# Kernel optimization log

Measured on AMD Instinct MI355X. Metric: run time of the kernel, lower is better.

The kernel has to match this reference:

```python
import jax, jax.numpy as jnp
import numpy as np

N, E, G = 20000, 200000, 32
D, H, C, L = 384, 12, 32, 6
NUM_RBF = 100
RBF_MIN, RBF_MAX = 0.0, 30.0


def _layer_norm(x, g, b, eps=1e-5):
    mu = jnp.mean(x, axis=-1, keepdims=True)
    var = jnp.var(x, axis=-1, keepdims=True)
    return (x - mu) * jax.lax.rsqrt(var + eps) * g + b


def setup_inputs() -> dict:
    key = jax.random.key(0)
    ks = jax.random.split(key, 32)
    s = 0.05
    inp = {
        'x': jax.random.normal(ks[0], (N, 20), jnp.float32),
        'pos': jax.random.normal(ks[1], (N, 3), jnp.float32) * 10.0,
        'edge_index': jax.random.randint(ks[2], (2, E), 0, N),
        'batch': jnp.sort(jax.random.randint(ks[3], (N,), 0, G)),
        # node embedding: Linear(20,384) + LayerNorm
        'emb_W': jax.random.normal(ks[4], (20, D)) * s,
        'emb_b': jnp.zeros((D,)),
        'emb_g': jnp.ones((D,)),
        'emb_beta': jnp.zeros((D,)),
        # edge encoder: Linear(100,384), Linear(384,384), LayerNorm
        'eW1': jax.random.normal(ks[5], (NUM_RBF, D)) * s,
        'eb1': jnp.zeros((D,)),
        'eW2': jax.random.normal(ks[6], (D, D)) * s,
        'eb2': jnp.zeros((D,)),
        'e_g': jnp.ones((D,)),
        'e_beta': jnp.zeros((D,)),
        # 6 stacked GATv2 layers
        'Wl': jax.random.normal(ks[7], (L, D, D)) * s,
        'bl': jnp.zeros((L, D)),
        'Wr': jax.random.normal(ks[8], (L, D, D)) * s,
        'br': jnp.zeros((L, D)),
        'We': jax.random.normal(ks[9], (L, D, D)) * s,
        'att': jax.random.normal(ks[10], (L, H, C)) * s,
        'cb': jnp.zeros((L, D)),
        # BatchNorm (eval mode, running stats)
        'bn_g': 1.0 + jax.random.normal(ks[11], (L, D)) * 0.05,
        'bn_b': jax.random.normal(ks[12], (L, D)) * 0.05,
        'bn_m': jax.random.normal(ks[13], (L, D)) * 0.05,
        'bn_v': jax.random.uniform(ks[14], (L, D), minval=0.5, maxval=1.5),
        # pool combine + head
        'pW': jax.random.normal(ks[15], (2 * D, D)) * s,
        'pb': jnp.zeros((D,)),
        'hW1': jax.random.normal(ks[16], (D, D)) * s,
        'hb1': jnp.zeros((D,)),
        'hW2': jax.random.normal(ks[17], (D, D // 2)) * s,
        'hb2': jnp.zeros((D // 2,)),
        'hW3': jax.random.normal(ks[18], (D // 2, 1)) * s,
        'hb3': jnp.zeros((1,)),
    }
    return inp


def reference(x, pos, edge_index, batch, emb_W, emb_b, emb_g, emb_beta,
              eW1, eb1, eW2, eb2, e_g, e_beta,
              Wl, bl, Wr, br, We, att, cb, bn_g, bn_b, bn_m, bn_v,
              pW, pb, hW1, hb1, hW2, hb2, hW3, hb3):
    src, dst = edge_index[0], edge_index[1]

    # node embedding (dropout = identity in eval)
    h = jax.nn.silu(_layer_norm(x @ emb_W + emb_b, emb_g, emb_beta))  # (N, D)

    # RBF edge features
    centers = jnp.linspace(RBF_MIN, RBF_MAX, NUM_RBF)
    spacing = (RBF_MAX - RBF_MIN) / (NUM_RBF - 1)
    gamma = 1.0 / (spacing ** 2 + 1e-8)
    dist = jnp.linalg.norm(pos[src] - pos[dst], axis=-1, keepdims=True)  # (E, 1)
    rbf = jnp.exp(-gamma * (dist - centers) ** 2)  # (E, NUM_RBF)
    e = jax.nn.silu(rbf @ eW1 + eb1)
    e = _layer_norm(e @ eW2 + eb2, e_g, e_beta)  # (E, D)

    for i in range(L):
        identity = h
        xl = (h @ Wl[i] + bl[i]).reshape(N, H, C)
        xr = (h @ Wr[i] + br[i]).reshape(N, H, C)
        ee = (e @ We[i]).reshape(E, H, C)
        m = jax.nn.leaky_relu(xl[src] + xr[dst] + ee, 0.2)  # (E, H, C)
        logits = jnp.einsum('ehc,hc->eh', m, att[i])  # (E, H)
        smax = jax.ops.segment_max(logits, dst, num_segments=N)
        a = jnp.exp(logits - smax[dst])
        denom = jax.ops.segment_sum(a, dst, num_segments=N)
        a = a / (denom[dst] + 1e-16)
        msg = (xl[src] * a[:, :, None]).reshape(E, H * C)
        out = jax.ops.segment_sum(msg, dst, num_segments=N) + cb[i]  # (N, D)
        out = (out - bn_m[i]) * jax.lax.rsqrt(bn_v[i] + 1e-5) * bn_g[i] + bn_b[i]
        h = jax.nn.silu(out) + identity

    cnt = jax.ops.segment_sum(jnp.ones((N,), h.dtype), batch, num_segments=G)
    h_mean = jax.ops.segment_sum(h, batch, num_segments=G) / jnp.maximum(cnt, 1.0)[:, None]
    h_max = jax.ops.segment_max(h, batch, num_segments=G)
    hg = jnp.concatenate([h_mean, h_max], axis=-1)  # (G, 2D)
    hg = jax.nn.silu(hg @ pW + pb)
    hg = jax.nn.silu(hg @ hW1 + hb1)
    hg = jax.nn.silu(hg @ hW2 + hb2)
    return (hg @ hW3 + hb3).squeeze(-1)  # (G,)
```

## Files before the change

### kernel.cpp

```cpp
#include <hip/hip_runtime.h>
#include <hip/hip_bf16.h>
#include <math.h>

#define NN 20000
#define EE 200000
#define GG 32
#define DD 384
#define HH 12
#define CC 32
#define LL 6
#define NRBF 100
#define CHUNK 32768

typedef short s16x8 __attribute__((ext_vector_type(8)));
typedef float f32x4 __attribute__((ext_vector_type(4)));
typedef unsigned int u32;

__device__ __forceinline__ float siluf(float x) { return x / (1.f + __expf(-x)); }
__device__ __forceinline__ float bf2f(unsigned short u) {
    return __uint_as_float(((unsigned int)u) << 16);
}

__device__ __forceinline__ void atomicMaxF(float* addr, float val) {
    if (val >= 0.f) atomicMax((int*)addr, __float_as_int(val));
    else atomicMin((unsigned int*)addr, __float_as_uint(val));
}

__device__ __forceinline__ void gload16(const void* g, void* l) {
    __builtin_amdgcn_global_load_lds((const __attribute__((address_space(1))) u32*)g,
                                     (__attribute__((address_space(3))) u32*)l, 16, 0, 0);
}

__device__ __forceinline__ bool tile_decode(int NC, int nrows, int& rowt, int& col) {
    const int t = blockIdx.x;
    const int q = t >> 3;
    col = q % NC;
    rowt = (q / NC) * 8 + (t & 7);
    return rowt < nrows;
}

__global__ void EquivariantProteinGNN_45552423141948_kernel() {}

__device__ __forceinline__ void gemm_kloop(const __hip_bfloat16* __restrict__ A,
                                           const __hip_bfloat16* __restrict__ Bt,
                                           int M, int K, int m0, int n0,
                                           unsigned short* As, unsigned short* Bs,
                                           f32x4 (&acc)[4][4]) {
    char* AsB = (char*)As;
    char* BsB = (char*)Bs;
    const int t = threadIdx.x;
    const int w = t >> 6, l = t & 63;
    const int wr = w >> 1, wc = w & 1;

    const int seg0 = 2 * w, seg1 = seg0 + 1;
    const int r0s = seg0 * 16 + (l >> 2);
    const int r1s = seg1 * 16 + (l >> 2);
    const int cg0 = (l & 3) ^ ((r0s >> 1) & 3);
    const int cg1 = (l & 3) ^ ((r1s >> 1) & 3);
    const size_t aSrc0 = (size_t)min(m0 + r0s, M - 1) * K + cg0 * 8;
    const size_t aSrc1 = (size_t)min(m0 + r1s, M - 1) * K + cg1 * 8;
    const size_t bSrc0 = (size_t)(n0 + r0s) * K + cg0 * 8;
    const size_t bSrc1 = (size_t)(n0 + r1s) * K + cg1 * 8;
    unsigned short* AsW0 = As + seg0 * 512;
    unsigned short* AsW1 = As + seg1 * 512;
    unsigned short* BsW0 = Bs + seg0 * 512;
    unsigned short* BsW1 = Bs + seg1 * 512;

    int aoff[4], boff[4];
#pragma unroll
    for (int m = 0; m < 4; ++m) {
        const int row = wr * 64 + m * 16 + (l & 15);
        aoff[m] = row * 64 + ((((l >> 4)) ^ ((row >> 1) & 3)) << 4);
        const int rowb = wc * 64 + m * 16 + (l & 15);
        boff[m] = rowb * 64 + ((((l >> 4)) ^ ((rowb >> 1) & 3)) << 4);
    }

    for (int kk = 0; kk < K; kk += 32) {
        __syncthreads();
        gload16(A + aSrc0 + kk, AsW0);
        gload16(A + aSrc1 + kk, AsW1);
        gload16(Bt + bSrc0 + kk, BsW0);
        gload16(Bt + bSrc1 + kk, BsW1);
        __syncthreads();
        s16x8 af[4], bfr[4];
#pragma unroll
        for (int m = 0; m < 4; ++m) af[m] = *(const s16x8*)(AsB + aoff[m]);
#pragma unroll
        for (int n = 0; n < 4; ++n) bfr[n] = *(const s16x8*)(BsB + boff[n]);
#pragma unroll
        for (int m = 0; m < 4; ++m)
#pragma unroll
            for (int n = 0; n < 4; ++n)
                acc[m][n] = __builtin_amdgcn_mfma_f32_16x16x32_bf16(af[m], bfr[n], acc[m][n], 0, 0, 0);
    }
}

template<bool BIAS, bool SILU>
__global__ __launch_bounds__(256) void k_gemm_bt(const __hip_bfloat16* __restrict__ A,
                                                 const __hip_bfloat16* __restrict__ Bt,
                                                 const float* __restrict__ bias,
                                                 __hip_bfloat16* __restrict__ Cmat,
                                                 int M, int N, int K) {
    int rowt, colt;
    if (!tile_decode(N >> 7, (M + 127) >> 7, rowt, colt)) return;
    const int m0 = rowt << 7, n0 = colt << 7;

    __shared__ unsigned short As[128 * 32];
    __shared__ unsigned short Bs[128 * 32];
    const int l = threadIdx.x & 63;
    const int w = threadIdx.x >> 6;
    const int wr = w >> 1, wc = w & 1;

    f32x4 acc[4][4] = {};
    gemm_kloop(A, Bt, M, K, m0, n0, As, Bs, acc);

#pragma unroll
    for (int n = 0; n < 4; ++n) {
        const int col = n0 + wc * 64 + n * 16 + (l & 15);
        const float bv = BIAS ? bias[col] : 0.f;
#pragma unroll
        for (int m = 0; m < 4; ++m) {
            const int rbase = m0 + wr * 64 + m * 16 + ((l >> 4) << 2);
#pragma unroll
            for (int r = 0; r < 4; ++r) {
                const int row = rbase + r;
                if (row < M) {
                    float v = acc[m][n][r] + bv;
                    if (SILU) v = siluf(v);
                    Cmat[(size_t)row * N + col] = __float2bfloat16(v);
                }
            }
        }
    }
}

__global__ __launch_bounds__(256) void k_gemm_attn(const __hip_bfloat16* __restrict__ A,
                                                   const __hip_bfloat16* __restrict__ Bt,
                                                   const __hip_bfloat16* __restrict__ xlr,
                                                   const int* __restrict__ src_p,
                                                   const int* __restrict__ dst_p,
                                                   const float* __restrict__ att_i,
                                                   float* __restrict__ logits,
                                                   int M, int K) {
    int rowt, colt;
    if (!tile_decode(DD >> 7, (M + 127) >> 7, rowt, colt)) return;
    const int m0 = rowt << 7, n0 = colt << 7;

    __shared__ char smem[16384];
    unsigned short* As = (unsigned short*)smem;
    unsigned short* Bs = (unsigned short*)(smem + 8192);
    const int l = threadIdx.x & 63;
    const int w = threadIdx.x >> 6;
    const int wr = w >> 1, wc = w & 1;

    f32x4 acc[4][4] = {};
    gemm_kloop(A, Bt, M, K, m0, n0, As, Bs, acc);

    __syncthreads();

    float* ep = (float*)(smem + w * 4096);
    const int row_l = l >> 2;
    const int c0 = (l & 3) << 4;
    const int gcol = n0 + wc * 64 + c0;
    const int hbase = (n0 + wc * 64) >> 5;
    const int rswz = row_l << 2;

    float attv[16];
#pragma unroll
    for (int k = 0; k < 4; ++k)
        *(float4*)(attv + 4 * k) = *(const float4*)(att_i + gcol + 4 * k);

#pragma unroll
    for (int m = 0; m < 4; ++m) {
        const int growu = m0 + wr * 64 + m * 16 + row_l;
        const int grow = min(growu, M - 1);
        const int s = src_p[grow], d = dst_p[grow];
        const uint4 vl0 = *(const uint4*)(xlr + (size_t)s * 768 + gcol);
        const uint4 vl1 = *(const uint4*)(xlr + (size_t)s * 768 + gcol + 8);
        const uint4 vr0 = *(const uint4*)(xlr + (size_t)d * 768 + 384 + gcol);
        const uint4 vr1 = *(const uint4*)(xlr + (size_t)d * 768 + 384 + gcol + 8);

#pragma unroll
        for (int n = 0; n < 4; ++n)
#pragma unroll
            for (int r = 0; r < 4; ++r) {
                const int row = ((l >> 4) << 2) + r;
                const int col = (n << 4) + (l & 15);
                ep[(row << 6) + (col ^ (row << 2))] = acc[m][n][r];
            }
        float av[16];
#pragma unroll
        for (int k = 0; k < 4; ++k) {
            const int sc0 = (c0 + (k << 2)) ^ rswz;
            *(f32x4*)(av + 4 * k) = *(const f32x4*)(ep + (row_l << 6) + sc0);
        }
        const u32 lw[8] = {vl0.x, vl0.y, vl0.z, vl0.w, vl1.x, vl1.y, vl1.z, vl1.w};
        const u32 rw[8] = {vr0.x, vr0.y, vr0.z, vr0.w, vr1.x, vr1.y, vr1.z, vr1.w};
        float part = 0.f;
#pragma unroll
        for (int q = 0; q < 8; ++q) {
            float v0 = av[2 * q] + bf2f((unsigned short)(lw[q] & 0xffff)) +
                       bf2f((unsigned short)(rw[q] & 0xffff));
            float v1 = av[2 * q + 1] + bf2f((unsigned short)(lw[q] >> 16)) +
                       bf2f((unsigned short)(rw[q] >> 16));
            v0 = (v0 > 0.f) ? v0 : 0.2f * v0;
            v1 = (v1 > 0.f) ? v1 : 0.2f * v1;
            part += v0 * attv[2 * q] + v1 * attv[2 * q + 1];
        }
        part += __shfl_xor(part, 1, 64);
        if (growu < M && (l & 1) == 0)
            logits[(size_t)growu * HH + hbase + ((l & 2) >> 1)] = part;
    }
}

__global__ void k_tw(const float* __restrict__ in, __hip_bfloat16* __restrict__ out, int nmat) {
    const size_t idx = (size_t)blockIdx.x * 256 + threadIdx.x;
    if (idx >= (size_t)nmat * DD * DD) return;
    const int m = idx / (DD * DD);
    const int rem = idx - (size_t)m * DD * DD;
    const int n = rem / DD, k = rem - n * DD;
    out[idx] = __float2bfloat16(in[(size_t)m * DD * DD + (size_t)k * DD + n]);
}

__global__ void k_twlr(const float* __restrict__ Wl, const float* __restrict__ Wr,
                       __hip_bfloat16* __restrict__ out) {
    const size_t idx = (size_t)blockIdx.x * 256 + threadIdx.x;
    if (idx >= (size_t)LL * 768 * DD) return;
    const int i = idx / (768 * DD);
    const int rem = idx - (size_t)i * 768 * DD;
    const int n = rem / DD, k = rem - n * DD;
    const float v = (n < DD) ? Wl[(size_t)i * DD * DD + (size_t)k * DD + n]
                             : Wr[(size_t)i * DD * DD + (size_t)k * DD + (n - DD)];
    out[idx] = __float2bfloat16(v);
}

__global__ void k_blr(const float* __restrict__ bl, const float* __restrict__ br,
                      float* __restrict__ blr) {
    const int idx = blockIdx.x * 256 + threadIdx.x;
    if (idx >= LL * 768) return;
    const int i = idx / 768, c = idx - i * 768;
    blr[idx] = (c < DD) ? bl[i * DD + c] : br[i * DD + c - DD];
}

__global__ void k_tw1(const float* __restrict__ in, __hip_bfloat16* __restrict__ out) {
    const int idx = blockIdx.x * 256 + threadIdx.x;
    if (idx >= DD * 128) return;
    const int n = idx >> 7, k = idx & 127;
    out[idx] = __float2bfloat16(k < NRBF ? in[(size_t)k * DD + n] : 0.f);
}

__global__ __launch_bounds__(256) void k_rbf_chunk(const float* __restrict__ pos,
                                                   const int* __restrict__ src_p,
                                                   const int* __restrict__ dst_p,
                                                   int e0, int cm,
                                                   __hip_bfloat16* __restrict__ rbfp) {
    const int el = blockIdx.x * 2 + (threadIdx.x >> 7);
    if (el >= cm) return;
    const int e = e0 + el;
    const int c = threadIdx.x & 127;
    const int s = src_p[e], d = dst_p[e];
    const float dx = pos[s * 3 + 0] - pos[d * 3 + 0];
    const float dy = pos[s * 3 + 1] - pos[d * 3 + 1];
    const float dz = pos[s * 3 + 2] - pos[d * 3 + 2];
    const float dist = sqrtf(dx * dx + dy * dy + dz * dz);
    const float spacing = 30.f / 99.f;
    const float gamma = 1.f / (spacing * spacing + 1e-8f);
    float v = 0.f;
    if (c < NRBF) {
        const float dd = dist - (float)c * spacing;
        v = __expf(-gamma * dd * dd);
    }
    rbfp[(size_t)el * 128 + c] = __float2bfloat16(v);
}

__global__ __launch_bounds__(512) void k_ln_rows(__hip_bfloat16* __restrict__ u,
                                                 const float* __restrict__ g,
                                                 const float* __restrict__ be) {
    const int w = threadIdx.x >> 6, l = threadIdx.x & 63;
    const int row = blockIdx.x * 8 + w;
    float vals[8];
    float s = 0.f, q = 0.f;
    if (l < 48) {
        const uint4 vu = *(const uint4*)(u + (size_t)row * DD + 8 * l);
        const unsigned int* uw = (const unsigned int*)&vu;
#pragma unroll
        for (int i = 0; i < 4; ++i) {
            vals[2 * i] = bf2f((unsigned short)(uw[i] & 0xffff));
            vals[2 * i + 1] = bf2f((unsigned short)(uw[i] >> 16));
        }
#pragma unroll
        for (int i = 0; i < 8; ++i) { s += vals[i]; q += vals[i] * vals[i]; }
    }
#pragma unroll
    for (int off = 1; off < 64; off <<= 1) {
        s += __shfl_xor(s, off, 64);
        q += __shfl_xor(q, off, 64);
    }
    const float mu = s / DD;
    const float rs = rsqrtf(q / DD - mu * mu + 1e-5f);
    if (l < 48) {
        unsigned int ow[4];
        const float4 g0 = *(const float4*)(g + 8 * l);
        const float4 g1 = *(const float4*)(g + 8 * l + 4);
        const float4 b0 = *(const float4*)(be + 8 * l);
        const float4 b1 = *(const float4*)(be + 8 * l + 4);
        const float gv[8] = {g0.x, g0.y, g0.z, g0.w, g1.x, g1.y, g1.z, g1.w};
        const float bv[8] = {b0.x, b0.y, b0.z, b0.w, b1.x, b1.y, b1.z, b1.w};
#pragma unroll
        for (int i = 0; i < 4; ++i) {
            const float y0 = (vals[2 * i] - mu) * rs * gv[2 * i] + bv[2 * i];
            const float y1 = (vals[2 * i + 1] - mu) * rs * gv[2 * i + 1] + bv[2 * i + 1];
            const unsigned short h0 = __bfloat16_as_ushort(__float2bfloat16(y0));
            const unsigned short h1 = __bfloat16_as_ushort(__float2bfloat16(y1));
            ow[i] = (unsigned int)h0 | ((unsigned int)h1 << 16);
        }
        *(uint4*)(u + (size_t)row * DD + 8 * l) = *(uint4*)ow;
    }
}

__global__ __launch_bounds__(384) void k_node_embed(const float* __restrict__ x,
                                                    const float* __restrict__ W,
                                                    const float* __restrict__ b,
                                                    const float* __restrict__ g,
                                                    const float* __restrict__ be,
                                                    float* __restrict__ h,
                                                    __hip_bfloat16* __restrict__ hb) {
    const int n = blockIdx.x, j = threadIdx.x;
    __shared__ float xrow[20];
    __shared__ float red[12];
    if (j < 20) xrow[j] = x[n * 20 + j];
    __syncthreads();
    float acc = b[j];
#pragma unroll
    for (int k = 0; k < 20; ++k) acc += xrow[k] * W[k * DD + j];
    float s = acc, q = acc * acc;
#pragma unroll
    for (int off = 32; off > 0; off >>= 1) {
        s += __shfl_down(s, off, 64);
        q += __shfl_down(q, off, 64);
    }
    const int wid = j >> 6;
    if ((j & 63) == 0) { red[wid] = s; red[6 + wid] = q; }
    __syncthreads();
    if (j == 0) {
        float ts = 0.f, tq = 0.f;
        for (int w = 0; w < 6; ++w) { ts += red[w]; tq += red[6 + w]; }
        float mu = ts / DD;
        red[0] = mu; red[6] = tq / DD - mu * mu;
    }
    __syncthreads();
    const float mu = red[0], var = red[6];
    float y = (acc - mu) * rsqrtf(var + 1e-5f) * g[j] + be[j];
    y = siluf(y);
    h[(size_t)n * DD + j] = y;
    hb[(size_t)n * DD + j] = __float2bfloat16(y);
}

__global__ void k_deg(const int* __restrict__ ei, int* __restrict__ deg) {
    int e = blockIdx.x * blockDim.x + threadIdx.x;
    if (e < EE) atomicAdd(&deg[ei[EE + e]], 1);
}

__global__ __launch_bounds__(1024) void k_scan(const int* __restrict__ deg, int* __restrict__ rp) {
    __shared__ int buf[1024];
    __shared__ int carry_s;
    const int tid = threadIdx.x;
    if (tid == 0) carry_s = 0;
    __syncthreads();
    for (int base = 0; base < NN; base += 1024) {
        int v = (base + tid < NN) ? deg[base + tid] : 0;
        buf[tid] = v;
        __syncthreads();
        for (int off = 1; off < 1024; off <<= 1) {
            int t = (tid >= off) ? buf[tid - off] : 0;
            __syncthreads();
            buf[tid] += t;
            __syncthreads();
        }
        const int incl = buf[tid];
        const int carry = carry_s;
        if (base + tid < NN) rp[base + tid] = carry + incl - v;
        __syncthreads();
        if (tid == 1023) carry_s = carry + incl;
        __syncthreads();
    }
    if (tid == 0) rp[NN] = carry_s;
}

__global__ void k_scatter(const int* __restrict__ ei, const int* __restrict__ rp,
                          int* __restrict__ cursor, int* __restrict__ col_e) {
    int e = blockIdx.x * blockDim.x + threadIdx.x;
    if (e < EE) {
        int d = ei[EE + e];
        int p = atomicAdd(&cursor[d], 1);
        col_e[rp[d] + p] = e;
    }
}

__global__ void k_perm(const int* __restrict__ ei, const int* __restrict__ col_e,
                       int* __restrict__ src_p, int* __restrict__ dst_p) {
    int p = blockIdx.x * blockDim.x + threadIdx.x;
    if (p < EE) {
        const int e = col_e[p];
        src_p[p] = ei[e];
        dst_p[p] = ei[EE + e];
    }
}

__global__ __launch_bounds__(256) void k_node_aggr(const float* __restrict__ logits,
                                                   const __hip_bfloat16* __restrict__ xlr,
                                                   const int* __restrict__ src_p,
                                                   const int* __restrict__ rp,
                                                   const float* __restrict__ cb_i,
                                                   const float* __restrict__ g_i,
                                                   const float* __restrict__ b_i,
                                                   const float* __restrict__ m_i,
                                                   const float* __restrict__ v_i,
                                                   float* __restrict__ h,
                                                   __hip_bfloat16* __restrict__ hb) {
    const int wv = threadIdx.x >> 6, l = threadIdx.x & 63;
    const int n = blockIdx.x * 4 + wv;
    if (n >= NN || l >= 48) return;
    const int beg = rp[n], end = rp[n + 1];
    const int head = l >> 2;
    const int j4 = l & 3;

    float mx = -INFINITY;
    for (int i = beg + j4; i < end; i += 4) mx = fmaxf(mx, logits[(size_t)i * HH + head]);
    mx = fmaxf(mx, __shfl_xor(mx, 1, 64));
    mx = fmaxf(mx, __shfl_xor(mx, 2, 64));
    float sum = 0.f;
    for (int i = beg + j4; i < end; i += 4) sum += __expf(logits[(size_t)i * HH + head] - mx);
    sum += __shfl_xor(sum, 1, 64);
    sum += __shfl_xor(sum, 2, 64);
    const float m_h = mx;
    const float inv_h = 1.f / (sum + 1e-16f);

    const int c0 = l * 8;
    float acc[8] = {};
    for (int i = beg; i < end; ++i) {
        const float a = __expf(logits[(size_t)i * HH + head] - m_h) * inv_h;
        const int s = src_p[i];
        const uint4 vx = *(const uint4*)(xlr + (size_t)s * 768 + c0);
        const u32* xw = (const u32*)&vx;
#pragma unroll
        for (int q = 0; q < 4; ++q) {
            acc[2 * q]     += bf2f((unsigned short)(xw[q] & 0xffff)) * a;
            acc[2 * q + 1] += bf2f((unsigned short)(xw[q] >> 16)) * a;
        }
    }
    const float4 cb0 = *(const float4*)(cb_i + c0), cb1 = *(const float4*)(cb_i + c0 + 4);
    const float4 gg0 = *(const float4*)(g_i + c0),  gg1 = *(const float4*)(g_i + c0 + 4);
    const float4 bb0 = *(const float4*)(b_i + c0),  bb1 = *(const float4*)(b_i + c0 + 4);
    const float4 mm0 = *(const float4*)(m_i + c0),  mm1 = *(const float4*)(m_i + c0 + 4);
    const float4 vv0 = *(const float4*)(v_i + c0),  vv1 = *(const float4*)(v_i + c0 + 4);
    const float cbv[8] = {cb0.x, cb0.y, cb0.z, cb0.w, cb1.x, cb1.y, cb1.z, cb1.w};
    const float gv[8]  = {gg0.x, gg0.y, gg0.z, gg0.w, gg1.x, gg1.y, gg1.z, gg1.w};
    const float bv[8]  = {bb0.x, bb0.y, bb0.z, bb0.w, bb1.x, bb1.y, bb1.z, bb1.w};
    const float mv[8]  = {mm0.x, mm0.y, mm0.z, mm0.w, mm1.x, mm1.y, mm1.z, mm1.w};
    const float vvv[8] = {vv0.x, vv0.y, vv0.z, vv0.w, vv1.x, vv1.y, vv1.z, vv1.w};
    float4 h0 = *(const float4*)(h + (size_t)n * DD + c0);
    float4 h1 = *(const float4*)(h + (size_t)n * DD + c0 + 4);
    float hv[8] = {h0.x, h0.y, h0.z, h0.w, h1.x, h1.y, h1.z, h1.w};
    unsigned int ow[4];
#pragma unroll
    for (int q = 0; q < 8; ++q) {
        float o = acc[q] + cbv[q];
        o = (o - mv[q]) * rsqrtf(vvv[q] + 1e-5f) * gv[q] + bv[q];
        hv[q] = siluf(o) + hv[q];
    }
#pragma unroll
    for (int q = 0; q < 4; ++q) {
        const unsigned short b0 = __bfloat16_as_ushort(__float2bfloat16(hv[2 * q]));
        const unsigned short b1 = __bfloat16_as_ushort(__float2bfloat16(hv[2 * q + 1]));
        ow[q] = (unsigned int)b0 | ((unsigned int)b1 << 16);
    }
    *(float4*)(h + (size_t)n * DD + c0) = make_float4(hv[0], hv[1], hv[2], hv[3]);
    *(float4*)(h + (size_t)n * DD + c0 + 4) = make_float4(hv[4], hv[5], hv[6], hv[7]);
    *(uint4*)(hb + (size_t)n * DD + c0) = *(uint4*)ow;
}

__global__ void k_fill(float* __restrict__ p, float v, int n) {
    int i = blockIdx.x * blockDim.x + threadIdx.x;
    if (i < n) p[i] = v;
}

__global__ __launch_bounds__(384) void k_pool2(const float* __restrict__ h,
                                               const int* __restrict__ batch,
                                               float* __restrict__ gsum,
                                               float* __restrict__ gmax,
                                               float* __restrict__ gcnt) {
    const int j = threadIdx.x;
    const int n0 = blockIdx.x * 256;
    const int n1 = min(n0 + 256, NN);
    int cur = batch[n0];
    float s = 0.f, mx = -INFINITY;
    int cnt = 0;
    for (int n = n0; n < n1; ++n) {
        const int g = batch[n];
        if (g != cur) {
            atomicAdd(&gsum[cur * DD + j], s);
            atomicMaxF(&gmax[cur * DD + j], mx);
            if (j == 0) atomicAdd(&gcnt[cur], (float)cnt);
            s = 0.f; mx = -INFINITY; cnt = 0; cur = g;
        }
        const float v = h[(size_t)n * DD + j];
        s += v; mx = fmaxf(mx, v); ++cnt;
    }
    atomicAdd(&gsum[cur * DD + j], s);
    atomicMaxF(&gmax[cur * DD + j], mx);
    if (j == 0) atomicAdd(&gcnt[cur], (float)cnt);
}

__global__ __launch_bounds__(384) void k_head(const float* __restrict__ gsum,
                                              const float* __restrict__ gmax,
                                              const float* __restrict__ gcnt,
                                              const float* __restrict__ pW,
                                              const float* __restrict__ pb,
                                              const float* __restrict__ hW1,
                                              const float* __restrict__ hb1,
                                              const float* __restrict__ hW2,
                                              const float* __restrict__ hb2,
                                              const float* __restrict__ hW3,
                                              const float* __restrict__ hb3,
                                              float* __restrict__ out) {
    const int g = blockIdx.x, j = threadIdx.x;
    __shared__ float hg[2 * DD];
    __shared__ float p1[DD];
    __shared__ float p2[DD];
    __shared__ float p3[DD / 2];
    __shared__ float red[6];
    const float cnt = fmaxf(gcnt[g], 1.f);
    hg[j] = gsum[g * DD + j] / cnt;
    hg[DD + j] = gmax[g * DD + j];
    __syncthreads();
    float a = pb[j];
    for (int k = 0; k < 2 * DD; ++k) a += hg[k] * pW[(size_t)k * DD + j];
    p1[j] = siluf(a);
    __syncthreads();
    a = hb1[j];
    for (int k = 0; k < DD; ++k) a += p1[k] * hW1[(size_t)k * DD + j];
    p2[j] = siluf(a);
    __syncthreads();
    if (j < DD / 2) {
        a = hb2[j];
        for (int k = 0; k < DD; ++k) a += p2[k] * hW2[(size_t)k * (DD / 2) + j];
        p3[j] = siluf(a);
    }
    __syncthreads();
    float v = (j < DD / 2) ? p3[j] * hW3[j] : 0.f;
#pragma unroll
    for (int off = 32; off > 0; off >>= 1) v += __shfl_down(v, off, 64);
    if ((j & 63) == 0) red[j >> 6] = v;
    __syncthreads();
    if (j == 0) {
        float s = 0.f;
        for (int w = 0; w < 6; ++w) s += red[w];
        out[g] = s + hb3[0];
    }
}

static inline int gemm_grid(int M, int N) {
    const int nr = (M + 127) >> 7, nc = N >> 7;
    return ((nr + 7) >> 3) * nc * 8;
}

extern "C" void kernel_launch(void* const* d_in, const int* in_sizes, int n_in,
                              void* d_out, int out_size, void* d_ws, size_t ws_size,
                              hipStream_t stream) {
    (void)in_sizes; (void)n_in; (void)out_size; (void)ws_size;
    const float* x      = (const float*)d_in[0];
    const float* pos    = (const float*)d_in[1];
    const int*   ei     = (const int*)d_in[2];
    const int*   batch  = (const int*)d_in[3];
    const float* emb_W  = (const float*)d_in[4];
    const float* emb_b  = (const float*)d_in[5];
    const float* emb_g  = (const float*)d_in[6];
    const float* emb_be = (const float*)d_in[7];
    const float* eW1    = (const float*)d_in[8];
    const float* eb1    = (const float*)d_in[9];
    const float* eW2    = (const float*)d_in[10];
    const float* eb2    = (const float*)d_in[11];
    const float* e_g    = (const float*)d_in[12];
    const float* e_be   = (const float*)d_in[13];
    const float* Wl     = (const float*)d_in[14];
    const float* bl     = (const float*)d_in[15];
    const float* Wr     = (const float*)d_in[16];
    const float* br     = (const float*)d_in[17];
    const float* We     = (const float*)d_in[18];
    const float* att    = (const float*)d_in[19];
    const float* cb     = (const float*)d_in[20];
    const float* bn_g   = (const float*)d_in[21];
    const float* bn_b   = (const float*)d_in[22];
    const float* bn_m   = (const float*)d_in[23];
    const float* bn_v   = (const float*)d_in[24];
    const float* pW     = (const float*)d_in[25];
    const float* pb     = (const float*)d_in[26];
    const float* hW1    = (const float*)d_in[27];
    const float* hb1    = (const float*)d_in[28];
    const float* hW2    = (const float*)d_in[29];
    const float* hb2    = (const float*)d_in[30];
    const float* hW3    = (const float*)d_in[31];
    const float* hb3    = (const float*)d_in[32];

    char* wp = (char*)d_ws;
    auto carve = [&](size_t bytes) -> void* {
        void* p = (void*)wp;
        wp += (bytes + 255) & ~(size_t)255;
        return p;
    };
    float* h      = (float*)carve((size_t)NN * DD * 4);
    __hip_bfloat16* hbf = (__hip_bfloat16*)carve((size_t)NN * DD * 2);
    __hip_bfloat16* xlr = (__hip_bfloat16*)carve((size_t)NN * 768 * 2);
    __hip_bfloat16* ebf = (__hip_bfloat16*)carve((size_t)EE * DD * 2);
    float* logits = (float*)carve((size_t)EE * HH * 4);
    int* deg      = (int*)carve((size_t)NN * 4);
    int* cursor   = (int*)carve((size_t)NN * 4);
    int* rp       = (int*)carve((size_t)(NN + 1) * 4);
    int* col_e    = (int*)carve((size_t)EE * 4);
    int* src_p    = (int*)carve((size_t)EE * 4);
    int* dst_p    = (int*)carve((size_t)EE * 4);
    float* gsum   = (float*)carve((size_t)GG * DD * 4);
    float* gmax   = (float*)carve((size_t)GG * DD * 4);
    float* gcnt   = (float*)carve((size_t)GG * 4);
    __hip_bfloat16* Wlrt = (__hip_bfloat16*)carve((size_t)LL * 768 * DD * 2);
    __hip_bfloat16* Wet  = (__hip_bfloat16*)carve((size_t)LL * DD * DD * 2);
    float* blr    = (float*)carve((size_t)LL * 768 * 4);
    __hip_bfloat16* eW1t = (__hip_bfloat16*)carve((size_t)DD * 128 * 2);
    __hip_bfloat16* eW2t = (__hip_bfloat16*)carve((size_t)DD * DD * 2);

    __hip_bfloat16* rbfc = (__hip_bfloat16*)logits;
    __hip_bfloat16* tc   = xlr;

    hipMemsetAsync(deg, 0, (size_t)NN * 4, stream);
    hipMemsetAsync(cursor, 0, (size_t)NN * 4, stream);

    {
        const int nblkLR = (int)(((size_t)LL * 768 * DD + 255) / 256);
        const int nblk6 = (int)(((size_t)LL * DD * DD + 255) / 256);
        k_twlr<<<nblkLR, 256, 0, stream>>>(Wl, Wr, Wlrt);
        k_tw<<<nblk6, 256, 0, stream>>>(We, Wet, LL);
        k_blr<<<(LL * 768 + 255) / 256, 256, 0, stream>>>(bl, br, blr);
        k_tw<<<(DD * DD + 255) / 256, 256, 0, stream>>>(eW2, eW2t, 1);
        k_tw1<<<(DD * 128 + 255) / 256, 256, 0, stream>>>(eW1, eW1t);
    }

    k_node_embed<<<NN, 384, 0, stream>>>(x, emb_W, emb_b, emb_g, emb_be, h, hbf);

    k_deg<<<(EE + 255) / 256, 256, 0, stream>>>(ei, deg);
    k_scan<<<1, 1024, 0, stream>>>(deg, rp);
    k_scatter<<<(EE + 255) / 256, 256, 0, stream>>>(ei, rp, cursor, col_e);
    k_perm<<<(EE + 255) / 256, 256, 0, stream>>>(ei, col_e, src_p, dst_p);

    for (int c0 = 0; c0 < EE; c0 += CHUNK) {
        const int cm = (EE - c0 < CHUNK) ? (EE - c0) : CHUNK;
        k_rbf_chunk<<<(cm + 1) / 2, 256, 0, stream>>>(pos, src_p, dst_p, c0, cm, rbfc);
        k_gemm_bt<true, true><<<gemm_grid(cm, DD), 256, 0, stream>>>(rbfc, eW1t, eb1, tc, cm, DD, 128);
        k_gemm_bt<true, false><<<gemm_grid(cm, DD), 256, 0, stream>>>(tc, eW2t, eb2,
                                                                      ebf + (size_t)c0 * DD, cm, DD, DD);
    }
    k_ln_rows<<<EE / 8, 512, 0, stream>>>(ebf, e_g, e_be);

    for (int i = 0; i < LL; ++i) {
        const __hip_bfloat16* Wlrt_i = Wlrt + (size_t)i * 768 * DD;
        const __hip_bfloat16* Wet_i  = Wet + (size_t)i * DD * DD;
        const float* blr_i = blr + (size_t)i * 768;
        const float* att_i = att + (size_t)i * HH * CC;
        const float* cb_i  = cb + (size_t)i * DD;
        const float* bng_i = bn_g + (size_t)i * DD;
        const float* bnb_i = bn_b + (size_t)i * DD;
        const float* bnm_i = bn_m + (size_t)i * DD;
        const float* bnv_i = bn_v + (size_t)i * DD;

        k_gemm_bt<true, false><<<gemm_grid(NN, 768), 256, 0, stream>>>(hbf, Wlrt_i, blr_i, xlr,
                                                                       NN, 768, DD);
        k_gemm_attn<<<gemm_grid(EE, DD), 256, 0, stream>>>(ebf, Wet_i, xlr, src_p, dst_p,
                                                           att_i, logits, EE, DD);
        k_node_aggr<<<(NN + 3) / 4, 256, 0, stream>>>(logits, xlr, src_p, rp, cb_i, bng_i, bnb_i,
                                                      bnm_i, bnv_i, h, hbf);
    }

    hipMemsetAsync(gsum, 0, (size_t)GG * DD * 4, stream);
    hipMemsetAsync(gcnt, 0, (size_t)GG * 4, stream);
    k_fill<<<(GG * DD + 255) / 256, 256, 0, stream>>>(gmax, -INFINITY, GG * DD);
    k_pool2<<<(NN + 255) / 256, 384, 0, stream>>>(h, batch, gsum, gmax, gcnt);
    k_head<<<GG, 384, 0, stream>>>(gsum, gmax, gcnt, pW, pb, hW1, hb1, hW2, hb2, hW3, hb3,
                                   (float*)d_out);
}
```

Before: 1.842 ms.

## Fuse RBF expansion into first edge-encoder GEMM A-tile generation

Removes the separate RBF kernel and its bf16 intermediate buffer. The new GEMM kernel computes each edge's distance and Gaussian basis values directly into the swizzled shared-memory A tile while B loads through global_load_lds, then applies bias and SiLU. The chunk size also grows from 32768 to 40000, so there are fewer chunk iterations and launches. The cost is redundant exp work across the three column tiles that share the same rows, and the larger chunk needs a bigger scratch buffer in xlr, which holds 20000*768 entries and so still fits.

```diff
diff --git a/kernel.cpp b/kernel.cpp
--- a/kernel.cpp
+++ b/kernel.cpp
@@ -10,7 +10,7 @@
 #define CC 32
 #define LL 6
 #define NRBF 100
-#define CHUNK 32768
+#define CHUNK 40000
 
 typedef short s16x8 __attribute__((ext_vector_type(8)));
 typedef float f32x4 __attribute__((ext_vector_type(4)));
@@ -134,6 +134,120 @@
     }
 }
 
+__global__ __launch_bounds__(256) void k_gemm_rbf(const float* __restrict__ pos,
+                                                  const int* __restrict__ src_p,
+                                                  const int* __restrict__ dst_p,
+                                                  int e0, int cm,
+                                                  const __hip_bfloat16* __restrict__ Bt,
+                                                  const float* __restrict__ bias,
+                                                  __hip_bfloat16* __restrict__ Cmat) {
+    int rowt, colt;
+    if (!tile_decode(DD >> 7, (cm + 127) >> 7, rowt, colt)) return;
+    const int m0 = rowt << 7, n0 = colt << 7;
+
+    __shared__ unsigned short As[128 * 32];
+    __shared__ unsigned short Bs[128 * 32];
+    char* AsB = (char*)As;
+    char* BsB = (char*)Bs;
+    const int t = threadIdx.x;
+    const int w = t >> 6, l = t & 63;
+    const int wr = w >> 1, wc = w & 1;
+
+    const float spacing = 30.f / 99.f;
+    const float gamma = 1.f / (spacing * spacing + 1e-8f);
+
+    const int rA0 = t >> 2, rA1 = 64 + (t >> 2);
+    const int sc = t & 3;
+    const int cgA0 = sc ^ ((rA0 >> 1) & 3);
+    const int cgA1 = sc ^ ((rA1 >> 1) & 3);
+    float distA[2];
+#pragma unroll
+    for (int i = 0; i < 2; ++i) {
+        const int row = i ? rA1 : rA0;
+        const int e = e0 + min(m0 + row, cm - 1);
+        const int sN = src_p[e], dN = dst_p[e];
+        const float dx = pos[sN * 3 + 0] - pos[dN * 3 + 0];
+        const float dy = pos[sN * 3 + 1] - pos[dN * 3 + 1];
+        const float dz = pos[sN * 3 + 2] - pos[dN * 3 + 2];
+        distA[i] = sqrtf(dx * dx + dy * dy + dz * dz);
+    }
+
+    const int seg0 = 2 * w, seg1 = seg0 + 1;
+    const int r0s = seg0 * 16 + (l >> 2);
+    const int r1s = seg1 * 16 + (l >> 2);
+    const int cgB0 = (l & 3) ^ ((r0s >> 1) & 3);
+    const int cgB1 = (l & 3) ^ ((r1s >> 1) & 3);
+    const size_t bSrc0 = (size_t)(n0 + r0s) * 128 + cgB0 * 8;
+    const size_t bSrc1 = (size_t)(n0 + r1s) * 128 + cgB1 * 8;
+    unsigned short* BsW0 = Bs + seg0 * 512;
+    unsigned short* BsW1 = Bs + seg1 * 512;
+
+    int aoff[4], boff[4];
+#pragma unroll
+    for (int m = 0; m < 4; ++m) {
+        const int row = wr * 64 + m * 16 + (l & 15);
+        aoff[m] = row * 64 + ((((l >> 4)) ^ ((row >> 1) & 3)) << 4);
+        const int rowb = wc * 64 + m * 16 + (l & 15);
+        boff[m] = rowb * 64 + ((((l >> 4)) ^ ((rowb >> 1) & 3)) << 4);
+    }
+
+    f32x4 acc[4][4] = {};
+
+    for (int kk = 0; kk < 128; kk += 32) {
+        __syncthreads();
+        gload16(Bt + bSrc0 + kk, BsW0);
+        gload16(Bt + bSrc1 + kk, BsW1);
+        uint4 pk[2];
+#pragma unroll
+        for (int i = 0; i < 2; ++i) {
+            const int kb = kk + (i ? cgA1 : cgA0) * 8;
+            const float dist = distA[i];
+            u32 w4[4];
+#pragma unroll
+            for (int j = 0; j < 4; ++j) {
+                const int k0 = kb + 2 * j, k1 = k0 + 1;
+                const float d0 = dist - (float)k0 * spacing;
+                const float d1 = dist - (float)k1 * spacing;
+                const float f0 = (k0 < NRBF) ? __expf(-gamma * d0 * d0) : 0.f;
+                const float f1 = (k1 < NRBF) ? __expf(-gamma * d1 * d1) : 0.f;
+                w4[j] = (u32)__bfloat16_as_ushort(__float2bfloat16(f0)) |
+                        ((u32)__bfloat16_as_ushort(__float2bfloat16(f1)) << 16);
+            }
+            pk[i] = make_uint4(w4[0], w4[1], w4[2], w4[3]);
+        }
+        *(uint4*)(AsB + t * 16) = pk[0];
+        *(uint4*)(AsB + 4096 + t * 16) = pk[1];
+        __syncthreads();
+        s16x8 af[4], bfr[4];
+#pragma unroll
+        for (int m = 0; m < 4; ++m) af[m] = *(const s16x8*)(AsB + aoff[m]);
+#pragma unroll
+        for (int n = 0; n < 4; ++n) bfr[n] = *(const s16x8*)(BsB + boff[n]);
+#pragma unroll
+        for (int m = 0; m < 4; ++m)
+#pragma unroll
+            for (int n = 0; n < 4; ++n)
+                acc[m][n] = __builtin_amdgcn_mfma_f32_16x16x32_bf16(af[m], bfr[n], acc[m][n], 0, 0, 0);
+    }
+
+#pragma unroll
+    for (int n = 0; n < 4; ++n) {
+        const int col = n0 + wc * 64 + n * 16 + (l & 15);
+        const float bv = bias[col];
+#pragma unroll
+        for (int m = 0; m < 4; ++m) {
+            const int rbase = m0 + wr * 64 + m * 16 + ((l >> 4) << 2);
+#pragma unroll
+            for (int r = 0; r < 4; ++r) {
+                const int row = rbase + r;
+                if (row < cm) {
+                    Cmat[(size_t)row * DD + col] = __float2bfloat16(siluf(acc[m][n][r] + bv));
+                }
+            }
+        }
+    }
+}
+
 __global__ __launch_bounds__(256) void k_gemm_attn(const __hip_bfloat16* __restrict__ A,
                                                    const __hip_bfloat16* __restrict__ Bt,
                                                    const __hip_bfloat16* __restrict__ xlr,
@@ -247,30 +361,6 @@
     if (idx >= DD * 128) return;
     const int n = idx >> 7, k = idx & 127;
     out[idx] = __float2bfloat16(k < NRBF ? in[(size_t)k * DD + n] : 0.f);
-}
-
-__global__ __launch_bounds__(256) void k_rbf_chunk(const float* __restrict__ pos,
-                                                   const int* __restrict__ src_p,
-                                                   const int* __restrict__ dst_p,
-                                                   int e0, int cm,
-                                                   __hip_bfloat16* __restrict__ rbfp) {
-    const int el = blockIdx.x * 2 + (threadIdx.x >> 7);
-    if (el >= cm) return;
-    const int e = e0 + el;
-    const int c = threadIdx.x & 127;
-    const int s = src_p[e], d = dst_p[e];
-    const float dx = pos[s * 3 + 0] - pos[d * 3 + 0];
-    const float dy = pos[s * 3 + 1] - pos[d * 3 + 1];
-    const float dz = pos[s * 3 + 2] - pos[d * 3 + 2];
-    const float dist = sqrtf(dx * dx + dy * dy + dz * dz);
-    const float spacing = 30.f / 99.f;
-    const float gamma = 1.f / (spacing * spacing + 1e-8f);
-    float v = 0.f;
-    if (c < NRBF) {
-        const float dd = dist - (float)c * spacing;
-        v = __expf(-gamma * dd * dd);
-    }
-    rbfp[(size_t)el * 128 + c] = __float2bfloat16(v);
 }
 
 __global__ __launch_bounds__(512) void k_ln_rows(__hip_bfloat16* __restrict__ u,
@@ -629,8 +719,7 @@
     __hip_bfloat16* eW1t = (__hip_bfloat16*)carve((size_t)DD * 128 * 2);
     __hip_bfloat16* eW2t = (__hip_bfloat16*)carve((size_t)DD * DD * 2);
 
-    __hip_bfloat16* rbfc = (__hip_bfloat16*)logits;
-    __hip_bfloat16* tc   = xlr;
+    __hip_bfloat16* tc = xlr;
 
     hipMemsetAsync(deg, 0, (size_t)NN * 4, stream);
     hipMemsetAsync(cursor, 0, (size_t)NN * 4, stream);
@@ -654,8 +743,8 @@
 
     for (int c0 = 0; c0 < EE; c0 += CHUNK) {
         const int cm = (EE - c0 < CHUNK) ? (EE - c0) : CHUNK;
-        k_rbf_chunk<<<(cm + 1) / 2, 256, 0, stream>>>(pos, src_p, dst_p, c0, cm, rbfc);
-        k_gemm_bt<true, true><<<gemm_grid(cm, DD), 256, 0, stream>>>(rbfc, eW1t, eb1, tc, cm, DD, 128);
+        k_gemm_rbf<<<gemm_grid(cm, DD), 256, 0, stream>>>(pos, src_p, dst_p, c0, cm,
+                                                          eW1t, eb1, tc);
         k_gemm_bt<true, false><<<gemm_grid(cm, DD), 256, 0, stream>>>(tc, eW2t, eb2,
                                                                       ebf + (size_t)c0 * DD, cm, DD, DD);
     }
```

After: 1.775 ms. 1.04x faster.
